# Kernel optimization log

Hardware: AMD Instinct MI355X
Metric: run time of the kernel (lower is better)

Reference implementation:

```python
import jax, jax.numpy as jnp
import numpy as np


def _nn_idx(query, ref):
    """Index of nearest ref point for each query point.
    query: [B,N,3], ref: [B,M,3] -> idx [B,N] (int32).
    Squared distance via ||q||^2 - 2 q.r + ||r||^2 (matches cdist+top1).
    """
    d2 = (jnp.sum(query * query, axis=-1, keepdims=True)
          - 2.0 * jnp.einsum('bnd,bmd->bnm', query, ref)
          + jnp.sum(ref * ref, axis=-1)[:, None, :])
    return jnp.argmin(d2, axis=-1)


def setup_inputs() -> dict:
    key = jax.random.key(0)
    k1, k2, k3 = jax.random.split(key, 3)
    B, N, M = 1, 16384, 16384  # batch hard-coded to 1 in original loops
    pred = jax.random.normal(k1, (B, N, 3), dtype=jnp.float32)
    gt = jax.random.normal(k2, (B, M, 3), dtype=jnp.float32)
    weight = jax.random.uniform(k3, (1,), dtype=jnp.float32)
    return {"pred": pred, "gt": gt, "weight": weight}


def reference(pred, gt, weight):
    # get_mse_loss2: weighted bidirectional nearest-neighbor MSE.
    w = weight[0]
    # B2A: align each pred point to its nearest gt point
    idx = _nn_idx(pred, gt)                                   # [B,N]
    align_gt = jnp.take_along_axis(gt, idx[..., None], axis=1)  # [B,N,3]
    B2A = jnp.mean((pred - align_gt) ** 2)
    # A2B: align each gt point to its nearest pred point
    idx2 = _nn_idx(gt, pred)                                  # [B,M]
    align_out = jnp.take_along_axis(pred, idx2[..., None], axis=1)  # [B,M,3]
    A2B = jnp.mean((align_out - gt) ** 2)
    return B2A * w + A2B * (1.0 - w)
```

## Files before the change

### kernel.cpp

```cpp
#include <hip/hip_runtime.h>


#define NPTS   16384
#define QBLK   256
#define QCH    (NPTS / QBLK)
#define SSPLIT 8
#define RBLK   (NPTS / SSPLIT)
#define NB1    (2 * QCH * SSPLIT)

typedef __attribute__((ext_vector_type(8)))  __bf16 bf16x8;
typedef __attribute__((ext_vector_type(16))) float  floatx16;

union frag16 { __bf16 v[16]; uint4 q[2]; };

__global__ __launch_bounds__(256) void prep_kernel(
    const float* __restrict__ pred, const float* __restrict__ gt,
    uint4* __restrict__ aform, uint4* __restrict__ bform,
    float* __restrict__ out)
{
    const int i = blockIdx.x * 256 + threadIdx.x;
    if (i == 0) out[0] = 0.0f;
    const int role = (i < NPTS) ? 0 : 1;
    const int p = i - role * NPTS;
    const float* __restrict__ src = role ? gt : pred;

    const float x = src[p * 3 + 0], y = src[p * 3 + 1], z = src[p * 3 + 2];
    const float nn = x * x + y * y + z * z;
    const __bf16 xh = (__bf16)x, yh = (__bf16)y, zh = (__bf16)z;
    const __bf16 xl = (__bf16)(x - (float)xh);
    const __bf16 yl = (__bf16)(y - (float)yh);
    const __bf16 zl = (__bf16)(z - (float)zh);
    const __bf16 nh = (__bf16)nn;
    const __bf16 nl = (__bf16)(nn - (float)nh);
    const __bf16 one = (__bf16)1.0f;

    frag16 A;
    A.v[0]  = (__bf16)(-2.0f * (float)xh); A.v[1]  = A.v[0];
    A.v[2]  = (__bf16)(-2.0f * (float)xl); A.v[3]  = A.v[2];
    A.v[4]  = (__bf16)(-2.0f * (float)yh); A.v[5]  = A.v[4];
    A.v[6]  = (__bf16)(-2.0f * (float)yl); A.v[7]  = A.v[6];
    A.v[8]  = (__bf16)(-2.0f * (float)zh); A.v[9]  = A.v[8];
    A.v[10] = (__bf16)(-2.0f * (float)zl); A.v[11] = A.v[10];
    A.v[12] = nh;  A.v[13] = nl;  A.v[14] = one;  A.v[15] = one;

    frag16 B;
    B.v[0] = xh;  B.v[1]  = xl;  B.v[2]  = xh;  B.v[3]  = xl;
    B.v[4] = yh;  B.v[5]  = yl;  B.v[6]  = yh;  B.v[7]  = yl;
    B.v[8] = zh;  B.v[9]  = zl;  B.v[10] = zh;  B.v[11] = zl;
    B.v[12] = one; B.v[13] = one; B.v[14] = nh;  B.v[15] = nl;

    uint4* da = aform + (size_t)role * (NPTS * 2)
              + ((p >> 5) * 64 + (p & 31));
    da[0]  = A.q[0];
    da[32] = A.q[1];
    uint4* db = bform + (size_t)role * (NPTS * 2) + p * 2;
    db[0] = B.q[0];
    db[1] = B.q[1];
}

#define MFMA_MIN_BLOCK(BQ, M)                                               \
    asm volatile(                                                           \
        "v_mfma_f32_32x32x16_bf16 v[32:47], %[A0], %[B], %[Z]\n\t"          \
        "v_mfma_f32_32x32x16_bf16 v[48:63], %[A1], %[B], %[Z]\n\t"          \
        "s_nop 7\n\ts_nop 7\n\ts_nop 7\n\ts_nop 7\n\t"                      \
        "v_min3_f32 %[M0],  %[M0],  v32, v48\n\t"                           \
        "v_min3_f32 %[M1],  %[M1],  v33, v49\n\t"                           \
        "v_min3_f32 %[M2],  %[M2],  v34, v50\n\t"                           \
        "v_min3_f32 %[M3],  %[M3],  v35, v51\n\t"                           \
        "v_min3_f32 %[M4],  %[M4],  v36, v52\n\t"                           \
        "v_min3_f32 %[M5],  %[M5],  v37, v53\n\t"                           \
        "v_min3_f32 %[M6],  %[M6],  v38, v54\n\t"                           \
        "v_min3_f32 %[M7],  %[M7],  v39, v55\n\t"                           \
        "v_min3_f32 %[M8],  %[M8],  v40, v56\n\t"                           \
        "v_min3_f32 %[M9],  %[M9],  v41, v57\n\t"                           \
        "v_min3_f32 %[M10], %[M10], v42, v58\n\t"                           \
        "v_min3_f32 %[M11], %[M11], v43, v59\n\t"                           \
        "v_min3_f32 %[M12], %[M12], v44, v60\n\t"                           \
        "v_min3_f32 %[M13], %[M13], v45, v61\n\t"                           \
        "v_min3_f32 %[M14], %[M14], v46, v62\n\t"                           \
        "v_min3_f32 %[M15], %[M15], v47, v63"                               \
        : [M0] "+v"(M[0]),  [M1] "+v"(M[1]),  [M2] "+v"(M[2]),              \
          [M3] "+v"(M[3]),  [M4] "+v"(M[4]),  [M5] "+v"(M[5]),              \
          [M6] "+v"(M[6]),  [M7] "+v"(M[7]),  [M8] "+v"(M[8]),              \
          [M9] "+v"(M[9]),  [M10] "+v"(M[10]), [M11] "+v"(M[11]),           \
          [M12] "+v"(M[12]), [M13] "+v"(M[13]), [M14] "+v"(M[14]),          \
          [M15] "+v"(M[15])                                                 \
        : [A0] "v"(a0), [A1] "v"(a1), [B] "v"(BQ), [Z] "v"(zero)            \
        : "v32", "v33", "v34", "v35", "v36", "v37", "v38", "v39",           \
          "v40", "v41", "v42", "v43", "v44", "v45", "v46", "v47",           \
          "v48", "v49", "v50", "v51", "v52", "v53", "v54", "v55",           \
          "v56", "v57", "v58", "v59", "v60", "v61", "v62", "v63")

__global__ __launch_bounds__(256) void nn_part_kernel(
    const uint4* __restrict__ aform, const uint4* __restrict__ bform,
    float* __restrict__ partial)
{
    const int bx   = blockIdx.x;
    const int dir  = bx >> 9;
    const int qc   = (bx & 511) >> 3;
    const int s    = bx & 7;
    const int tid  = threadIdx.x;
    const int lane = tid & 63;
    const int wave = tid >> 6;
    const int lid  = lane & 31;
    const int half = lane >> 5;

    const uint4* __restrict__ Aref = aform + (size_t)(dir ? 0 : 1) * (NPTS * 2);
    const uint4* __restrict__ Bqry = bform + (size_t)(dir ? 1 : 0) * (NPTS * 2);

    const int qbase = qc * QBLK + wave * 64;
    const bf16x8 bq0 = __builtin_bit_cast(bf16x8, Bqry[(qbase + lid) * 2 + half]);
    const bf16x8 bq1 = __builtin_bit_cast(bf16x8, Bqry[(qbase + 32 + lid) * 2 + half]);

    floatx16 zero;
#pragma unroll
    for (int k = 0; k < 16; ++k) zero[k] = 0.0f;

    float ma[16], mb[16];
#pragma unroll
    for (int k = 0; k < 16; ++k) { ma[k] = 3.4e38f; mb[k] = 3.4e38f; }

    const uint4* gp = Aref + (size_t)s * (RBLK * 2) + half * 32 + lid;
#pragma unroll 2
    for (int t = 0; t < RBLK / 32; t += 2) {
        const bf16x8 a0 = __builtin_bit_cast(bf16x8, gp[t * 64]);
        const bf16x8 a1 = __builtin_bit_cast(bf16x8, gp[t * 64 + 64]);
        MFMA_MIN_BLOCK(bq0, ma);
        MFMA_MIN_BLOCK(bq1, mb);
    }

    float* pout = partial + ((size_t)((dir * QCH + qc) * SSPLIT + s)) * QBLK
                + wave * 64;
    {
        float a = fminf(fminf(ma[0], ma[1]), fminf(ma[2], ma[3]));
        float b = fminf(fminf(ma[4], ma[5]), fminf(ma[6], ma[7]));
        float c = fminf(fminf(ma[8], ma[9]), fminf(ma[10], ma[11]));
        float d = fminf(fminf(ma[12], ma[13]), fminf(ma[14], ma[15]));
        float v = fminf(fminf(a, b), fminf(c, d));
        v = fminf(v, __shfl_xor(v, 32));
        if (half == 0) pout[lid] = v;
    }
    {
        float a = fminf(fminf(mb[0], mb[1]), fminf(mb[2], mb[3]));
        float b = fminf(fminf(mb[4], mb[5]), fminf(mb[6], mb[7]));
        float c = fminf(fminf(mb[8], mb[9]), fminf(mb[10], mb[11]));
        float d = fminf(fminf(mb[12], mb[13]), fminf(mb[14], mb[15]));
        float v = fminf(fminf(a, b), fminf(c, d));
        v = fminf(v, __shfl_xor(v, 32));
        if (half == 0) pout[32 + lid] = v;
    }
}

__global__ __launch_bounds__(256) void nn_combine_kernel(
    const float* __restrict__ partial, const float* __restrict__ weight,
    float* __restrict__ out)
{
    const int b   = blockIdx.x;
    const int dir = b >> 6;
    const int qc  = b & 63;
    const int t   = threadIdx.x;

    const float* p = partial + ((size_t)((dir * QCH + qc) * SSPLIT)) * QBLK;
    float v = p[t];
#pragma unroll
    for (int s = 1; s < SSPLIT; ++s)
        v = fminf(v, p[s * QBLK + t]);

    for (int off = 32; off; off >>= 1) v += __shfl_down(v, off);
    __shared__ float ws[4];
    if ((t & 63) == 0) ws[t >> 6] = v;
    __syncthreads();
    if (t == 0) {
        const float sum = ws[0] + ws[1] + ws[2] + ws[3];
        const float wgt = weight[0];
        const float scale = (dir ? (1.0f - wgt) : wgt) / (3.0f * (float)NPTS);
        atomicAdd(out, sum * scale);
    }
}

extern "C" void kernel_launch(void* const* d_in, const int* in_sizes, int n_in,
                              void* d_out, int out_size, void* d_ws, size_t ws_size,
                              hipStream_t stream) {
    const float* pred   = (const float*)d_in[0];
    const float* gt     = (const float*)d_in[1];
    const float* weight = (const float*)d_in[2];

    float* partial = (float*)d_ws;
    uint4* aform = (uint4*)((char*)d_ws + (size_t)2 * QCH * SSPLIT * QBLK * 4);
    uint4* bform = aform + (size_t)2 * NPTS * 2;

    prep_kernel<<<2 * NPTS / 256, 256, 0, stream>>>(pred, gt, aform, bform,
                                                    (float*)d_out);
    nn_part_kernel<<<NB1, 256, 0, stream>>>(aform, bform, partial);
    nn_combine_kernel<<<2 * QCH, 256, 0, stream>>>(partial, weight, (float*)d_out);
}
```

Measured before the change: 81.17 us.

## Software-pipeline reference fragment loads with a 4-stage asm register ring

Replaces the compiler-scheduled global loads of reference fragments with hand-written inline-asm loads into four fixed register buffers (v64–v95). Loads are issued several stages ahead and gated by s_waitcnt vmcnt(6), so memory latency overlaps with the MFMA and min3 work. The aim is to remove load stalls in the inner distance-min loop. In exchange it pins 32 extra VGPRs, prefetches past the end of each reference slice into adjacent workspace memory, and relies on manual waitcnt bookkeeping staying correct.

Measured after the change: 82.22 us. No clear change (+1.3%).

```diff
diff --git a/kernel.cpp b/kernel.cpp
--- a/kernel.cpp
+++ b/kernel.cpp
@@ -58,10 +58,10 @@
     db[1] = B.q[1];
 }
 
-#define MFMA_MIN_BLOCK(BQ, M)                                               \
+#define MMB(A0S, A1S, BQ, M)                                                \
     asm volatile(                                                           \
-        "v_mfma_f32_32x32x16_bf16 v[32:47], %[A0], %[B], %[Z]\n\t"          \
-        "v_mfma_f32_32x32x16_bf16 v[48:63], %[A1], %[B], %[Z]\n\t"          \
+        "v_mfma_f32_32x32x16_bf16 v[32:47], " A0S ", %[B], %[Z]\n\t"        \
+        "v_mfma_f32_32x32x16_bf16 v[48:63], " A1S ", %[B], %[Z]\n\t"        \
         "s_nop 7\n\ts_nop 7\n\ts_nop 7\n\ts_nop 7\n\t"                      \
         "v_min3_f32 %[M0],  %[M0],  v32, v48\n\t"                           \
         "v_min3_f32 %[M1],  %[M1],  v33, v49\n\t"                           \
@@ -85,11 +85,27 @@
           [M9] "+v"(M[9]),  [M10] "+v"(M[10]), [M11] "+v"(M[11]),           \
           [M12] "+v"(M[12]), [M13] "+v"(M[13]), [M14] "+v"(M[14]),          \
           [M15] "+v"(M[15])                                                 \
-        : [A0] "v"(a0), [A1] "v"(a1), [B] "v"(BQ), [Z] "v"(zero)            \
+        : [B] "v"(BQ), [Z] "v"(zero)                                        \
         : "v32", "v33", "v34", "v35", "v36", "v37", "v38", "v39",           \
           "v40", "v41", "v42", "v43", "v44", "v45", "v46", "v47",           \
           "v48", "v49", "v50", "v51", "v52", "v53", "v54", "v55",           \
           "v56", "v57", "v58", "v59", "v60", "v61", "v62", "v63")
+
+#define ISSUE(D0S, D1S, C0, C1, C2, C3, C4, C5, C6, C7)                     \
+    asm volatile(                                                           \
+        "global_load_dwordx4 " D0S ", %[off], %[base]\n\t"                  \
+        "global_load_dwordx4 " D1S ", %[off], %[base] offset:1024\n\t"      \
+        "v_add_u32 %[off], 0x800, %[off]"                                   \
+        : [off] "+v"(voff)                                                  \
+        : [base] "s"(abase)                                                 \
+        : C0, C1, C2, C3, C4, C5, C6, C7, "memory")
+
+#define ISSUE0 ISSUE("v[64:67]", "v[68:71]", "v64","v65","v66","v67","v68","v69","v70","v71")
+#define ISSUE1 ISSUE("v[72:75]", "v[76:79]", "v72","v73","v74","v75","v76","v77","v78","v79")
+#define ISSUE2 ISSUE("v[80:83]", "v[84:87]", "v80","v81","v82","v83","v84","v85","v86","v87")
+#define ISSUE3 ISSUE("v[88:91]", "v[92:95]", "v88","v89","v90","v91","v92","v93","v94","v95")
+
+#define WAIT6 asm volatile("s_waitcnt vmcnt(6)" ::: "memory")
 
 __global__ __launch_bounds__(256) void nn_part_kernel(
     const uint4* __restrict__ aform, const uint4* __restrict__ bform,
@@ -120,14 +136,23 @@
 #pragma unroll
     for (int k = 0; k < 16; ++k) { ma[k] = 3.4e38f; mb[k] = 3.4e38f; }
 
-    const uint4* gp = Aref + (size_t)s * (RBLK * 2) + half * 32 + lid;
-#pragma unroll 2
-    for (int t = 0; t < RBLK / 32; t += 2) {
-        const bf16x8 a0 = __builtin_bit_cast(bf16x8, gp[t * 64]);
-        const bf16x8 a1 = __builtin_bit_cast(bf16x8, gp[t * 64 + 64]);
-        MFMA_MIN_BLOCK(bq0, ma);
-        MFMA_MIN_BLOCK(bq1, mb);
-    }
+    asm volatile("s_waitcnt vmcnt(0)" ::: "memory");
+
+    const uint4* abase = Aref + (size_t)s * (RBLK * 2);
+    unsigned voff = (unsigned)((half * 32 + lid) * 16);
+    ISSUE0; ISSUE1; ISSUE2; ISSUE3;
+
+    for (int j = 0; j < 8; ++j) {
+        WAIT6; MMB("v[64:67]", "v[68:71]", bq0, ma);
+               MMB("v[64:67]", "v[68:71]", bq1, mb); ISSUE0;
+        WAIT6; MMB("v[72:75]", "v[76:79]", bq0, ma);
+               MMB("v[72:75]", "v[76:79]", bq1, mb); ISSUE1;
+        WAIT6; MMB("v[80:83]", "v[84:87]", bq0, ma);
+               MMB("v[80:83]", "v[84:87]", bq1, mb); ISSUE2;
+        WAIT6; MMB("v[88:91]", "v[92:95]", bq0, ma);
+               MMB("v[88:91]", "v[92:95]", bq1, mb); ISSUE3;
+    }
+    asm volatile("s_waitcnt vmcnt(0)" ::: "memory");
 
     float* pout = partial + ((size_t)((dir * QCH + qc) * SSPLIT + s)) * QBLK
                 + wave * 64;
```

## Stage reference fragments in double-buffered LDS shared across waves

Applied to the files above, without the earlier changes.

All four waves of a block now load the reference MFMA A-fragments cooperatively into a double-buffered shared-memory tile, instead of each wave reading the same fragments from global memory. Prefetches for the next round are held in registers during compute and written to the other buffer before a barrier. This cuts redundant global and L2 traffic, but adds LDS reads, block-wide barriers and extra register pressure.

New measurement: 81.23 us. About the same (+0.1%).

```diff
diff --git a/kernel.cpp b/kernel.cpp
--- a/kernel.cpp
+++ b/kernel.cpp
@@ -120,13 +120,48 @@
 #pragma unroll
     for (int k = 0; k < 16; ++k) { ma[k] = 3.4e38f; mb[k] = 3.4e38f; }
 
-    const uint4* gp = Aref + (size_t)s * (RBLK * 2) + half * 32 + lid;
-#pragma unroll 2
-    for (int t = 0; t < RBLK / 32; t += 2) {
-        const bf16x8 a0 = __builtin_bit_cast(bf16x8, gp[t * 64]);
-        const bf16x8 a1 = __builtin_bit_cast(bf16x8, gp[t * 64 + 64]);
-        MFMA_MIN_BLOCK(bq0, ma);
-        MFMA_MIN_BLOCK(bq1, mb);
+    __shared__ uint4 sbuf[2][16 * 64];
+    const uint4* abase = Aref + (size_t)s * (RBLK * 2);
+
+    {
+        const uint4* g = abase + (4 * wave) * 64 + lane;
+        uint4* d = &sbuf[0][(4 * wave) * 64 + lane];
+        d[0]   = g[0];
+        d[64]  = g[64];
+        d[128] = g[128];
+        d[192] = g[192];
+    }
+    __syncthreads();
+
+    for (int r = 0; r < 4; ++r) {
+        const int b = r & 1;
+
+        uint4 st0, st1, st2, st3;
+        if (r < 3) {
+            const uint4* g = abase + ((r + 1) * 16 + 4 * wave) * 64 + lane;
+            st0 = g[0];
+            st1 = g[64];
+            st2 = g[128];
+            st3 = g[192];
+        }
+
+        const uint4* sb = &sbuf[b][lane];
+#pragma unroll
+        for (int j = 0; j < 8; ++j) {
+            const bf16x8 a0 = __builtin_bit_cast(bf16x8, sb[(2 * j) * 64]);
+            const bf16x8 a1 = __builtin_bit_cast(bf16x8, sb[(2 * j + 1) * 64]);
+            MFMA_MIN_BLOCK(bq0, ma);
+            MFMA_MIN_BLOCK(bq1, mb);
+        }
+
+        if (r < 3) {
+            uint4* d = &sbuf[b ^ 1][(4 * wave) * 64 + lane];
+            d[0]   = st0;
+            d[64]  = st1;
+            d[128] = st2;
+            d[192] = st3;
+        }
+        __syncthreads();
     }
 
     float* pout = partial + ((size_t)((dir * QCH + qc) * SSPLIT + s)) * QBLK
```

## Batch four MFMAs per hazard wait and double the reference split count

Applied to the files above, without the earlier changes.

Fuses the two per-query-group MFMA+min blocks into one asm block that issues four MFMAs before a single s_nop hazard wait, so the wait cost is amortized over twice the work. The accumulator input is now the inline constant 0 instead of a zero register vector. The second min accumulator lives in hard-coded VGPRs v96-v111 across asm statements, which relies on the compiler not reusing those registers between them. SSPLIT grows from 8 to 16 to launch more blocks, which doubles the partial buffer and the combine reads.

Measured after the change: 81.67 us. No clear change (+0.6%).

```diff
diff --git a/kernel.cpp b/kernel.cpp
--- a/kernel.cpp
+++ b/kernel.cpp
@@ -4,12 +4,11 @@
 #define NPTS   16384
 #define QBLK   256
 #define QCH    (NPTS / QBLK)
-#define SSPLIT 8
+#define SSPLIT 16
 #define RBLK   (NPTS / SSPLIT)
 #define NB1    (2 * QCH * SSPLIT)
 
 typedef __attribute__((ext_vector_type(8)))  __bf16 bf16x8;
-typedef __attribute__((ext_vector_type(16))) float  floatx16;
 
 union frag16 { __bf16 v[16]; uint4 q[2]; };
 
@@ -58,10 +57,12 @@
     db[1] = B.q[1];
 }
 
-#define MFMA_MIN_BLOCK(BQ, M)                                               \
+#define MMB4(A0, A1, BQ0, BQ1, M)                                           \
     asm volatile(                                                           \
-        "v_mfma_f32_32x32x16_bf16 v[32:47], %[A0], %[B], %[Z]\n\t"          \
-        "v_mfma_f32_32x32x16_bf16 v[48:63], %[A1], %[B], %[Z]\n\t"          \
+        "v_mfma_f32_32x32x16_bf16 v[32:47], %[a0], %[b0], 0\n\t"            \
+        "v_mfma_f32_32x32x16_bf16 v[48:63], %[a1], %[b0], 0\n\t"            \
+        "v_mfma_f32_32x32x16_bf16 v[64:79], %[a0], %[b1], 0\n\t"            \
+        "v_mfma_f32_32x32x16_bf16 v[80:95], %[a1], %[b1], 0\n\t"            \
         "s_nop 7\n\ts_nop 7\n\ts_nop 7\n\ts_nop 7\n\t"                      \
         "v_min3_f32 %[M0],  %[M0],  v32, v48\n\t"                           \
         "v_min3_f32 %[M1],  %[M1],  v33, v49\n\t"                           \
@@ -78,27 +79,49 @@
         "v_min3_f32 %[M12], %[M12], v44, v60\n\t"                           \
         "v_min3_f32 %[M13], %[M13], v45, v61\n\t"                           \
         "v_min3_f32 %[M14], %[M14], v46, v62\n\t"                           \
-        "v_min3_f32 %[M15], %[M15], v47, v63"                               \
+        "v_min3_f32 %[M15], %[M15], v47, v63\n\t"                           \
+        "v_min3_f32 v96,  v96,  v64, v80\n\t"                               \
+        "v_min3_f32 v97,  v97,  v65, v81\n\t"                               \
+        "v_min3_f32 v98,  v98,  v66, v82\n\t"                               \
+        "v_min3_f32 v99,  v99,  v67, v83\n\t"                               \
+        "v_min3_f32 v100, v100, v68, v84\n\t"                               \
+        "v_min3_f32 v101, v101, v69, v85\n\t"                               \
+        "v_min3_f32 v102, v102, v70, v86\n\t"                               \
+        "v_min3_f32 v103, v103, v71, v87\n\t"                               \
+        "v_min3_f32 v104, v104, v72, v88\n\t"                               \
+        "v_min3_f32 v105, v105, v73, v89\n\t"                               \
+        "v_min3_f32 v106, v106, v74, v90\n\t"                               \
+        "v_min3_f32 v107, v107, v75, v91\n\t"                               \
+        "v_min3_f32 v108, v108, v76, v92\n\t"                               \
+        "v_min3_f32 v109, v109, v77, v93\n\t"                               \
+        "v_min3_f32 v110, v110, v78, v94\n\t"                               \
+        "v_min3_f32 v111, v111, v79, v95"                                   \
         : [M0] "+v"(M[0]),  [M1] "+v"(M[1]),  [M2] "+v"(M[2]),              \
           [M3] "+v"(M[3]),  [M4] "+v"(M[4]),  [M5] "+v"(M[5]),              \
           [M6] "+v"(M[6]),  [M7] "+v"(M[7]),  [M8] "+v"(M[8]),              \
           [M9] "+v"(M[9]),  [M10] "+v"(M[10]), [M11] "+v"(M[11]),           \
           [M12] "+v"(M[12]), [M13] "+v"(M[13]), [M14] "+v"(M[14]),          \
           [M15] "+v"(M[15])                                                 \
-        : [A0] "v"(a0), [A1] "v"(a1), [B] "v"(BQ), [Z] "v"(zero)            \
+        : [a0] "v"(A0), [a1] "v"(A1), [b0] "v"(BQ0), [b1] "v"(BQ1)          \
         : "v32", "v33", "v34", "v35", "v36", "v37", "v38", "v39",           \
           "v40", "v41", "v42", "v43", "v44", "v45", "v46", "v47",           \
           "v48", "v49", "v50", "v51", "v52", "v53", "v54", "v55",           \
-          "v56", "v57", "v58", "v59", "v60", "v61", "v62", "v63")
+          "v56", "v57", "v58", "v59", "v60", "v61", "v62", "v63",           \
+          "v64", "v65", "v66", "v67", "v68", "v69", "v70", "v71",           \
+          "v72", "v73", "v74", "v75", "v76", "v77", "v78", "v79",           \
+          "v80", "v81", "v82", "v83", "v84", "v85", "v86", "v87",           \
+          "v88", "v89", "v90", "v91", "v92", "v93", "v94", "v95",           \
+          "v96", "v97", "v98", "v99", "v100", "v101", "v102", "v103",       \
+          "v104", "v105", "v106", "v107", "v108", "v109", "v110", "v111")
 
 __global__ __launch_bounds__(256) void nn_part_kernel(
     const uint4* __restrict__ aform, const uint4* __restrict__ bform,
     float* __restrict__ partial)
 {
     const int bx   = blockIdx.x;
-    const int dir  = bx >> 9;
-    const int qc   = (bx & 511) >> 3;
-    const int s    = bx & 7;
+    const int dir  = bx >> 10;
+    const int qc   = (bx >> 4) & 63;
+    const int s    = bx & 15;
     const int tid  = threadIdx.x;
     const int lane = tid & 63;
     const int wave = tid >> 6;
@@ -112,22 +135,47 @@
     const bf16x8 bq0 = __builtin_bit_cast(bf16x8, Bqry[(qbase + lid) * 2 + half]);
     const bf16x8 bq1 = __builtin_bit_cast(bf16x8, Bqry[(qbase + 32 + lid) * 2 + half]);
 
-    floatx16 zero;
+    float ma[16];
 #pragma unroll
-    for (int k = 0; k < 16; ++k) zero[k] = 0.0f;
-
-    float ma[16], mb[16];
-#pragma unroll
-    for (int k = 0; k < 16; ++k) { ma[k] = 3.4e38f; mb[k] = 3.4e38f; }
+    for (int k = 0; k < 16; ++k) ma[k] = 3.4e38f;
+
+    asm volatile(
+        "v_mov_b32 v96,  0x7F7FFFFF\n\tv_mov_b32 v97,  0x7F7FFFFF\n\t"
+        "v_mov_b32 v98,  0x7F7FFFFF\n\tv_mov_b32 v99,  0x7F7FFFFF\n\t"
+        "v_mov_b32 v100, 0x7F7FFFFF\n\tv_mov_b32 v101, 0x7F7FFFFF\n\t"
+        "v_mov_b32 v102, 0x7F7FFFFF\n\tv_mov_b32 v103, 0x7F7FFFFF\n\t"
+        "v_mov_b32 v104, 0x7F7FFFFF\n\tv_mov_b32 v105, 0x7F7FFFFF\n\t"
+        "v_mov_b32 v106, 0x7F7FFFFF\n\tv_mov_b32 v107, 0x7F7FFFFF\n\t"
+        "v_mov_b32 v108, 0x7F7FFFFF\n\tv_mov_b32 v109, 0x7F7FFFFF\n\t"
+        "v_mov_b32 v110, 0x7F7FFFFF\n\tv_mov_b32 v111, 0x7F7FFFFF"
+        ::: "v96", "v97", "v98", "v99", "v100", "v101", "v102", "v103",
+            "v104", "v105", "v106", "v107", "v108", "v109", "v110", "v111");
 
     const uint4* gp = Aref + (size_t)s * (RBLK * 2) + half * 32 + lid;
 #pragma unroll 2
     for (int t = 0; t < RBLK / 32; t += 2) {
         const bf16x8 a0 = __builtin_bit_cast(bf16x8, gp[t * 64]);
         const bf16x8 a1 = __builtin_bit_cast(bf16x8, gp[t * 64 + 64]);
-        MFMA_MIN_BLOCK(bq0, ma);
-        MFMA_MIN_BLOCK(bq1, mb);
-    }
+        MMB4(a0, a1, bq0, bq1, ma);
+    }
+
+    float mb[16];
+    asm volatile(
+        "v_mov_b32 %0,  v96\n\tv_mov_b32 %1,  v97\n\t"
+        "v_mov_b32 %2,  v98\n\tv_mov_b32 %3,  v99\n\t"
+        "v_mov_b32 %4,  v100\n\tv_mov_b32 %5,  v101\n\t"
+        "v_mov_b32 %6,  v102\n\tv_mov_b32 %7,  v103\n\t"
+        "v_mov_b32 %8,  v104\n\tv_mov_b32 %9,  v105\n\t"
+        "v_mov_b32 %10, v106\n\tv_mov_b32 %11, v107\n\t"
+        "v_mov_b32 %12, v108\n\tv_mov_b32 %13, v109\n\t"
+        "v_mov_b32 %14, v110\n\tv_mov_b32 %15, v111"
+        : "=v"(mb[0]), "=v"(mb[1]), "=v"(mb[2]), "=v"(mb[3]),
+          "=v"(mb[4]), "=v"(mb[5]), "=v"(mb[6]), "=v"(mb[7]),
+          "=v"(mb[8]), "=v"(mb[9]), "=v"(mb[10]), "=v"(mb[11]),
+          "=v"(mb[12]), "=v"(mb[13]), "=v"(mb[14]), "=v"(mb[15])
+        :
+        : "v96", "v97", "v98", "v99", "v100", "v101", "v102", "v103",
+          "v104", "v105", "v106", "v107", "v108", "v109", "v110", "v111");
 
     float* pout = partial + ((size_t)((dir * QCH + qc) * SSPLIT + s)) * QBLK
                 + wave * 64;
@@ -164,7 +212,7 @@
     float v = p[t];
 #pragma unroll
     for (int s = 1; s < SSPLIT; ++s)
-        v = fminf(v, p[s * QBLK + t]);
+        v = fminf(v, p[(size_t)s * QBLK + t]);
 
     for (int off = 32; off; off >>= 1) v += __shfl_down(v, off);
     __shared__ float ws[4];
```
